# Kernel tuning notes

Measured on AMD Instinct MI355X. Metric: run time of the kernel, lower is better.

Reference implementation:

```python
import jax, jax.numpy as jnp
from jax import lax
import numpy as np

IN_DIM, HID, B, T = 8, 50, 4096, 512

def setup_inputs() -> dict:
    key = jax.random.key(0)
    ks = jax.random.split(key, 8)
    s_ih = 1.0 / np.sqrt(HID)
    return {
        "x": jax.random.normal(ks[0], (B, T, IN_DIM), dtype=jnp.float32),
        "W_ih": jax.random.uniform(ks[1], (3 * HID, IN_DIM), jnp.float32, -s_ih, s_ih),
        "W_hh": jax.random.uniform(ks[2], (3 * HID, HID), jnp.float32, -s_ih, s_ih),
        "b_ih": jax.random.uniform(ks[3], (3 * HID,), jnp.float32, -s_ih, s_ih),
        "b_hh": jax.random.uniform(ks[4], (3 * HID,), jnp.float32, -s_ih, s_ih),
        "W_out": jax.random.uniform(ks[5], (1, HID), jnp.float32, -s_ih, s_ih),
        "b_out": jax.random.uniform(ks[6], (1,), jnp.float32, -s_ih, s_ih),
    }

def reference(x, W_ih, W_hh, b_ih, b_hh, W_out, b_out):
    # Precompute input projections for all timesteps: [B, T, 3H]
    xW = jnp.einsum('bti,gi->btg', x, W_ih) + b_ih

    def step(h, xw_t):  # h: [B, H], xw_t: [B, 3H]
        gi_r, gi_z, gi_n = jnp.split(xw_t, 3, axis=-1)
        gh = h @ W_hh.T + b_hh
        gh_r, gh_z, gh_n = jnp.split(gh, 3, axis=-1)
        r = jax.nn.sigmoid(gi_r + gh_r)
        z = jax.nn.sigmoid(gi_z + gh_z)
        n = jnp.tanh(gi_n + r * gh_n)
        h_new = (1.0 - z) * n + z * h
        return h_new, None

    h0 = jnp.zeros((x.shape[0], W_hh.shape[1]), dtype=x.dtype)
    hT, _ = lax.scan(step, h0, jnp.moveaxis(xW, 1, 0))  # scan over time
    # Linear head on final hidden state; torch squeezes the layer dim -> [B, 1]
    return hT @ W_out.T + b_out
```

## Files before the change

### kernel.cpp

```cpp
#include <hip/hip_runtime.h>

#define HID 50
#define IND 8
#define TLEN 512
#define NB 16
#define CH 128
#define XSTR 1032
#define BSTR 72
#define NTHR 512

typedef _Float16 f16x8 __attribute__((ext_vector_type(8)));
typedef _Float16 f16x4 __attribute__((ext_vector_type(4)));
typedef float f32x4 __attribute__((ext_vector_type(4)));

__global__ __launch_bounds__(NTHR, 1) void gru_mfma8(
    const float* __restrict__ x,
    const float* __restrict__ W_ih,
    const float* __restrict__ W_hh,
    const float* __restrict__ b_ih,
    const float* __restrict__ b_hh,
    const float* __restrict__ W_out,
    const float* __restrict__ b_out,
    float* __restrict__ out)
{
    const int tid  = threadIdx.x;
    const int wave = tid >> 6;
    const int lane = tid & 63;
    const int m16  = lane & 15;
    const int quad = lane >> 4;
    const int bb   = blockIdx.x;

    const int t0  = 2 * wave;
    const int t1  = 2 * wave + 1;
    const int jh0 = 4 * t0 + quad;
    const int jh1 = 4 * t1 + quad;

    __shared__ _Float16 x_lds[NB * XSTR];
    __shared__ _Float16 B_lds[2][16 * BSTR];
    __shared__ float    red[NB * 56];

    auto aval = [&](int tt, int k) -> float {
        const int R  = 16 * tt + m16;
        const int rj = R >> 2;
        const int g  = R & 3;
        if (rj >= HID) return 0.f;
        const float sc = (g <= 1) ? -1.44269504f : 2.88539008f;
        float w = 0.f;
        if (g <= 1) {
            if (k < HID)      w = W_hh[(g * HID + rj) * HID + k];
            else if (k >= 56) w = W_ih[(g * HID + rj) * IND + (k - 56)];
        } else if (g == 2) {
            if (k < HID)      w = W_hh[(2 * HID + rj) * HID + k];
        } else {
            if (k >= 56)      w = W_ih[(2 * HID + rj) * IND + (k - 56)];
        }
        return sc * w;
    };

    f16x8 a00, a01, a10, a11;
#pragma unroll
    for (int j = 0; j < 8; ++j) {
        a00[j] = (_Float16)aval(t0, quad * 8 + j);
        a01[j] = (_Float16)aval(t0, 32 + quad * 8 + j);
        a10[j] = (_Float16)aval(t1, quad * 8 + j);
        a11[j] = (_Float16)aval(t1, 32 + quad * 8 + j);
    }

    auto mkbias = [&](int jh) -> f32x4 {
        f32x4 b = {0.f, 0.f, 0.f, 0.f};
        if (jh < HID) {
            b[0] = -1.44269504f * (b_ih[jh] + b_hh[jh]);
            b[1] = -1.44269504f * (b_ih[HID + jh] + b_hh[HID + jh]);
            b[2] =  2.88539008f * b_hh[2 * HID + jh];
            b[3] =  2.88539008f * b_ih[2 * HID + jh];
        }
        return b;
    };
    const f32x4 bias0 = mkbias(jh0);
    const f32x4 bias1 = mkbias(jh1);

    float h0 = 0.f, h1 = 0.f;

    auto stage_chunk = [&](int c) {
        const int n = tid >> 5;
        const int s = tid & 31;
        const float4* src = (const float4*)(x + ((size_t)(bb * NB + n) * TLEN + (size_t)c * CH) * IND);
#pragma unroll
        for (int r2 = 0; r2 < 8; ++r2) {
            const int fidx = s + 32 * r2;
            const float4 v = src[fidx];
            const int trel = fidx >> 1;
            const int d    = (fidx & 1) * 4;
            *(f16x4*)&x_lds[n * XSTR + trel * 8 + d] =
                f16x4{(_Float16)v.x, (_Float16)v.y, (_Float16)v.z, (_Float16)v.w};
        }
    };

    auto copy_x = [&](int trel, int buf) {
        *(unsigned*)&B_lds[buf][m16 * BSTR + 56 + 2 * quad] =
            *(const unsigned*)&x_lds[m16 * XSTR + trel * 8 + 2 * quad];
    };

    {
        _Float16* bz = &B_lds[0][0];
        for (int idx = tid; idx < 2 * 16 * BSTR; idx += NTHR)
            bz[idx] = (_Float16)0.f;
    }
    stage_chunk(0);
    __syncthreads();

    const int bq = m16 * BSTR + quad * 8;
    const int bw = m16 * BSTR;

    auto gates = [&](const f32x4& cc, float h) -> float {
        const float R2 = __builtin_amdgcn_exp2f(cc[0]);
        const float r  = __builtin_amdgcn_rcpf(1.0f + R2);
        const float Z2 = __builtin_amdgcn_exp2f(cc[1]);
        const float E  = __builtin_amdgcn_exp2f(cc[3] + r * cc[2]);
        const float num = E * (Z2 + h) + (h - Z2);
        const float den = (E + 1.0f) * (Z2 + 1.0f);
        return num * __builtin_amdgcn_rcpf(den);
    };

    for (int c = 0; c < 4; ++c) {
        if (c != 0) { stage_chunk(c); __syncthreads(); }
        if (wave == 7) copy_x(0, 0);
        __syncthreads();
#pragma unroll 4
        for (int i = 0; i < CH; i += 2) {
            if (wave == 7) {
                copy_x(i + 1, 1);
            } else {
                const f16x8 bf0 = *(const f16x8*)&B_lds[0][bq];
                const f16x8 bf1 = *(const f16x8*)&B_lds[0][bq + 32];
                f32x4 c0 = __builtin_amdgcn_mfma_f32_16x16x32_f16(a00, bf0, bias0, 0, 0, 0);
                f32x4 c1 = __builtin_amdgcn_mfma_f32_16x16x32_f16(a10, bf0, bias1, 0, 0, 0);
                c0 = __builtin_amdgcn_mfma_f32_16x16x32_f16(a01, bf1, c0, 0, 0, 0);
                c1 = __builtin_amdgcn_mfma_f32_16x16x32_f16(a11, bf1, c1, 0, 0, 0);
                h0 = gates(c0, h0);
                h1 = gates(c1, h1);
                B_lds[1][bw + jh0] = (_Float16)h0;
                B_lds[1][bw + jh1] = (_Float16)h1;
            }
            __syncthreads();
            if (wave == 7) {
                if (i + 2 < CH) copy_x(i + 2, 0);
            } else {
                const f16x8 bf0 = *(const f16x8*)&B_lds[1][bq];
                const f16x8 bf1 = *(const f16x8*)&B_lds[1][bq + 32];
                f32x4 c0 = __builtin_amdgcn_mfma_f32_16x16x32_f16(a00, bf0, bias0, 0, 0, 0);
                f32x4 c1 = __builtin_amdgcn_mfma_f32_16x16x32_f16(a10, bf0, bias1, 0, 0, 0);
                c0 = __builtin_amdgcn_mfma_f32_16x16x32_f16(a01, bf1, c0, 0, 0, 0);
                c1 = __builtin_amdgcn_mfma_f32_16x16x32_f16(a11, bf1, c1, 0, 0, 0);
                h0 = gates(c0, h0);
                h1 = gates(c1, h1);
                B_lds[0][bw + jh0] = (_Float16)h0;
                B_lds[0][bw + jh1] = (_Float16)h1;
            }
            __syncthreads();
        }
    }

    if (jh0 < HID) red[m16 * 56 + jh0] = h0 * W_out[jh0];
    if (jh1 < HID) red[m16 * 56 + jh1] = h1 * W_out[jh1];
    __syncthreads();
    if (tid < NB) {
        float s = b_out[0];
        for (int j = 0; j < HID; ++j) s += red[tid * 56 + j];
        out[bb * NB + tid] = s;
    }
}

extern "C" void kernel_launch(void* const* d_in, const int* in_sizes, int n_in,
                              void* d_out, int out_size, void* d_ws, size_t ws_size,
                              hipStream_t stream) {
    const float* x     = (const float*)d_in[0];
    const float* W_ih  = (const float*)d_in[1];
    const float* W_hh  = (const float*)d_in[2];
    const float* b_ih  = (const float*)d_in[3];
    const float* b_hh  = (const float*)d_in[4];
    const float* W_out = (const float*)d_in[5];
    const float* b_out = (const float*)d_in[6];
    float* out = (float*)d_out;

    const int B = in_sizes[0] / (TLEN * IND);
    gru_mfma8<<<B / NB, NTHR, 0, stream>>>(x, W_ih, W_hh, b_ih, b_hh, W_out, b_out, out);
}
```

Baseline: 242.1 us.

## Drop x-copy wave; read x fragments directly and pack hidden state in fragment layout

Removes the eighth wave that copied each timestep's input into the B operand buffer. The quad-3 lanes now load their second B fragment straight from a per-timestep x_frag array, staged in the MFMA fragment order. The hidden state is stored in a permuted fragment layout, with W rows permuted to match, so each lane writes its two outputs as one packed f16x2 store and reads B with contiguous 16-byte loads. This cuts per-step LDS traffic and the work in the barrier-bound recurrence, at the cost of a more intricate indexing scheme and a scattered staging write pattern.

```diff
diff --git a/kernel.cpp b/kernel.cpp
--- a/kernel.cpp
+++ b/kernel.cpp
@@ -5,15 +5,15 @@
 #define TLEN 512
 #define NB 16
 #define CH 128
-#define XSTR 1032
-#define BSTR 72
-#define NTHR 512
+#define XTS 136
+#define NTHR 448
 
 typedef _Float16 f16x8 __attribute__((ext_vector_type(8)));
 typedef _Float16 f16x4 __attribute__((ext_vector_type(4)));
+typedef _Float16 f16x2 __attribute__((ext_vector_type(2)));
 typedef float f32x4 __attribute__((ext_vector_type(4)));
 
-__global__ __launch_bounds__(NTHR, 1) void gru_mfma8(
+__global__ __launch_bounds__(NTHR, 1) void gru_mfma9(
     const float* __restrict__ x,
     const float* __restrict__ W_ih,
     const float* __restrict__ W_hh,
@@ -32,12 +32,14 @@
 
     const int t0  = 2 * wave;
     const int t1  = 2 * wave + 1;
-    const int jh0 = 4 * t0 + quad;
-    const int jh1 = 4 * t1 + quad;
+    const int jh0 = 8 * wave + quad;
+    const int jh1 = 8 * wave + 4 + quad;
 
-    __shared__ _Float16 x_lds[NB * XSTR];
-    __shared__ _Float16 B_lds[2][16 * BSTR];
+    __shared__ _Float16 B_lds[2 * 896];
+    __shared__ _Float16 x_frag[CH * XTS];
     __shared__ float    red[NB * 56];
+
+    const int P[8] = {0, 4, 1, 5, 2, 6, 3, 7};
 
     auto aval = [&](int tt, int k) -> float {
         const int R  = 16 * tt + m16;
@@ -59,11 +61,11 @@
 
     f16x8 a00, a01, a10, a11;
 #pragma unroll
-    for (int j = 0; j < 8; ++j) {
-        a00[j] = (_Float16)aval(t0, quad * 8 + j);
-        a01[j] = (_Float16)aval(t0, 32 + quad * 8 + j);
-        a10[j] = (_Float16)aval(t1, quad * 8 + j);
-        a11[j] = (_Float16)aval(t1, 32 + quad * 8 + j);
+    for (int p = 0; p < 8; ++p) {
+        a00[p] = (_Float16)aval(t0, quad * 8 + P[p]);
+        a01[p] = (_Float16)aval(t0, 32 + quad * 8 + P[p]);
+        a10[p] = (_Float16)aval(t1, quad * 8 + P[p]);
+        a11[p] = (_Float16)aval(t1, 32 + quad * 8 + P[p]);
     }
 
     auto mkbias = [&](int jh) -> f32x4 {
@@ -82,35 +84,27 @@
     float h0 = 0.f, h1 = 0.f;
 
     auto stage_chunk = [&](int c) {
-        const int n = tid >> 5;
-        const int s = tid & 31;
-        const float4* src = (const float4*)(x + ((size_t)(bb * NB + n) * TLEN + (size_t)c * CH) * IND);
-#pragma unroll
-        for (int r2 = 0; r2 < 8; ++r2) {
-            const int fidx = s + 32 * r2;
-            const float4 v = src[fidx];
-            const int trel = fidx >> 1;
-            const int d    = (fidx & 1) * 4;
-            *(f16x4*)&x_lds[n * XSTR + trel * 8 + d] =
-                f16x4{(_Float16)v.x, (_Float16)v.y, (_Float16)v.z, (_Float16)v.w};
+        for (int u = tid; u < NB * CH; u += NTHR) {
+            const int n    = u >> 7;
+            const int trel = u & (CH - 1);
+            const float4* s = (const float4*)(x + ((size_t)(bb * NB + n) * TLEN + (size_t)c * CH + trel) * IND);
+            const float4 va = s[0];
+            const float4 vb = s[1];
+            const f16x4 lo = {(_Float16)va.x, (_Float16)vb.x, (_Float16)va.y, (_Float16)vb.y};
+            const f16x4 hi = {(_Float16)va.z, (_Float16)vb.z, (_Float16)va.w, (_Float16)vb.w};
+            *(f16x4*)&x_frag[trel * XTS + n * 8]     = lo;
+            *(f16x4*)&x_frag[trel * XTS + n * 8 + 4] = hi;
         }
     };
 
-    auto copy_x = [&](int trel, int buf) {
-        *(unsigned*)&B_lds[buf][m16 * BSTR + 56 + 2 * quad] =
-            *(const unsigned*)&x_lds[m16 * XSTR + trel * 8 + 2 * quad];
-    };
-
-    {
-        _Float16* bz = &B_lds[0][0];
-        for (int idx = tid; idx < 2 * 16 * BSTR; idx += NTHR)
-            bz[idx] = (_Float16)0.f;
-    }
+    for (int idx = tid; idx < 2 * 896; idx += NTHR)
+        B_lds[idx] = (_Float16)0.f;
     stage_chunk(0);
     __syncthreads();
 
-    const int bq = m16 * BSTR + quad * 8;
-    const int bw = m16 * BSTR;
+    const int lane8 = lane * 8;
+    const _Float16* xq = &x_frag[m16 * 8];
+    const int wad = wave * 128 + m16 * 8 + 2 * quad;
 
     auto gates = [&](const f32x4& cc, float h) -> float {
         const float R2 = __builtin_amdgcn_exp2f(cc[0]);
@@ -122,42 +116,28 @@
         return num * __builtin_amdgcn_rcpf(den);
     };
 
+    auto step = [&](int i, int cur, int nxt) {
+        _Float16* Bc = &B_lds[cur * 896];
+        _Float16* Bn = &B_lds[nxt * 896];
+        const f16x8 bf0 = *(const f16x8*)(Bc + lane8);
+        const _Float16* p1 = (quad == 3) ? (xq + (size_t)i * XTS) : (Bc + 512 + lane8);
+        const f16x8 bf1 = *(const f16x8*)p1;
+        f32x4 c0 = __builtin_amdgcn_mfma_f32_16x16x32_f16(a00, bf0, bias0, 0, 0, 0);
+        f32x4 c1 = __builtin_amdgcn_mfma_f32_16x16x32_f16(a10, bf0, bias1, 0, 0, 0);
+        c0 = __builtin_amdgcn_mfma_f32_16x16x32_f16(a01, bf1, c0, 0, 0, 0);
+        c1 = __builtin_amdgcn_mfma_f32_16x16x32_f16(a11, bf1, c1, 0, 0, 0);
+        h0 = gates(c0, h0);
+        h1 = gates(c1, h1);
+        *(f16x2*)(Bn + wad) = f16x2{(_Float16)h0, (_Float16)h1};
+        __syncthreads();
+    };
+
     for (int c = 0; c < 4; ++c) {
         if (c != 0) { stage_chunk(c); __syncthreads(); }
-        if (wave == 7) copy_x(0, 0);
-        __syncthreads();
 #pragma unroll 4
         for (int i = 0; i < CH; i += 2) {
-            if (wave == 7) {
-                copy_x(i + 1, 1);
-            } else {
-                const f16x8 bf0 = *(const f16x8*)&B_lds[0][bq];
-                const f16x8 bf1 = *(const f16x8*)&B_lds[0][bq + 32];
-                f32x4 c0 = __builtin_amdgcn_mfma_f32_16x16x32_f16(a00, bf0, bias0, 0, 0, 0);
-                f32x4 c1 = __builtin_amdgcn_mfma_f32_16x16x32_f16(a10, bf0, bias1, 0, 0, 0);
-                c0 = __builtin_amdgcn_mfma_f32_16x16x32_f16(a01, bf1, c0, 0, 0, 0);
-                c1 = __builtin_amdgcn_mfma_f32_16x16x32_f16(a11, bf1, c1, 0, 0, 0);
-                h0 = gates(c0, h0);
-                h1 = gates(c1, h1);
-                B_lds[1][bw + jh0] = (_Float16)h0;
-                B_lds[1][bw + jh1] = (_Float16)h1;
-            }
-            __syncthreads();
-            if (wave == 7) {
-                if (i + 2 < CH) copy_x(i + 2, 0);
-            } else {
-                const f16x8 bf0 = *(const f16x8*)&B_lds[1][bq];
-                const f16x8 bf1 = *(const f16x8*)&B_lds[1][bq + 32];
-                f32x4 c0 = __builtin_amdgcn_mfma_f32_16x16x32_f16(a00, bf0, bias0, 0, 0, 0);
-                f32x4 c1 = __builtin_amdgcn_mfma_f32_16x16x32_f16(a10, bf0, bias1, 0, 0, 0);
-                c0 = __builtin_amdgcn_mfma_f32_16x16x32_f16(a01, bf1, c0, 0, 0, 0);
-                c1 = __builtin_amdgcn_mfma_f32_16x16x32_f16(a11, bf1, c1, 0, 0, 0);
-                h0 = gates(c0, h0);
-                h1 = gates(c1, h1);
-                B_lds[0][bw + jh0] = (_Float16)h0;
-                B_lds[0][bw + jh1] = (_Float16)h1;
-            }
-            __syncthreads();
+            step(i,     0, 1);
+            step(i + 1, 1, 0);
         }
     }
 
@@ -184,5 +164,5 @@
     float* out = (float*)d_out;
 
     const int B = in_sizes[0] / (TLEN * IND);
-    gru_mfma8<<<B / NB, NTHR, 0, stream>>>(x, W_ih, W_hh, b_ih, b_hh, W_out, b_out, out);
+    gru_mfma9<<<B / NB, NTHR, 0, stream>>>(x, W_ih, W_hh, b_ih, b_hh, W_out, b_out, out);
 }
```

After: 232.8 us (median of 2 runs). 3.8% less time.
